# Optimization experiments

Measured on AMD Instinct MI355X. Metric: run time of the kernel, lower is better.

Reference implementation:

```python
import jax, jax.numpy as jnp
import numpy as np

D_MODEL = 128
NUM_HEADS = 8
DEPTH = D_MODEL // NUM_HEADS
NEG = -1e9


def _dense_params(key, d_in, d_out):
    kw, kb = jax.random.split(key)
    # Glorot-uniform like keras Dense default
    lim = np.sqrt(6.0 / (d_in + d_out))
    w = jax.random.uniform(kw, (d_in, d_out), jnp.float32, -lim, lim)
    b = jnp.zeros((d_out,), jnp.float32)
    return w, b


def setup_inputs() -> dict:
    key = jax.random.key(0)
    ks = jax.random.split(key, 16)
    B, N, M, d = 256, 128, 128, D_MODEL
    inp = {
        'x_self': jax.random.normal(ks[0], (B, N, d), jnp.float32),
        'adj_self': jax.random.randint(ks[1], (B, N, N), 0, 2, jnp.int32),
        'mask_self': jnp.ones((B, N), jnp.int32),
        'x_cross': jax.random.normal(ks[2], (B, M, d), jnp.float32),
        'mask_cross': jnp.ones((B, M), jnp.int32),
    }
    names = ['wq_s', 'wk_s', 'wv_s', 'wo_s', 'wq_c', 'wk_c', 'wv_c', 'wo_c']
    for i, nm in enumerate(names):
        w, b = _dense_params(ks[3 + i], d, d)
        inp[nm] = w
        inp['b' + nm[1:]] = b
    wg, bg = _dense_params(ks[12], 3 * d, d)
    inp['wg'] = wg
    inp['bg'] = bg
    return inp


def _split_heads(x):
    B, N, _ = x.shape
    return x.reshape(B, N, NUM_HEADS, DEPTH).transpose(0, 2, 1, 3)  # [B,H,N,depth]


def _merge_heads(x):
    B, H, N, Dp = x.shape
    return x.transpose(0, 2, 1, 3).reshape(B, N, H * Dp)


def _attention(q, k, v, mask, adj=None):
    # q,k,v: [B,H,Nq,depth]; mask: [B,Nk]; adj: [B,Nq,Nk] or None
    logits = jnp.einsum('bhqd,bhkd->bhqk', q, k) / jnp.sqrt(jnp.float32(DEPTH))
    if adj is not None:
        logits = logits + ((1.0 - adj.astype(jnp.float32)) * NEG)[:, None, :, :]
    logits = logits + ((1.0 - mask.astype(jnp.float32)) * NEG)[:, None, None, :]
    w = jax.nn.softmax(logits, axis=-1)
    return jnp.einsum('bhqk,bhkd->bhqd', w, v)


def reference(x_self, adj_self, mask_self, x_cross, mask_cross,
              wq_s, bq_s, wk_s, bk_s, wv_s, bv_s, wo_s, bo_s,
              wq_c, bq_c, wk_c, bk_c, wv_c, bv_c, wo_c, bo_c,
              wg, bg):
    # Self attention (adjacency + padding mask)
    q_s = _split_heads(x_self @ wq_s + bq_s)
    k_s = _split_heads(x_self @ wk_s + bk_s)
    v_s = _split_heads(x_self @ wv_s + bv_s)
    out_s = _merge_heads(_attention(q_s, k_s, v_s, mask_self, adj_self)) @ wo_s + bo_s
    # Cross attention (padding mask only); dropout inactive at inference
    q_c = _split_heads(x_self @ wq_c + bq_c)
    k_c = _split_heads(x_cross @ wk_c + bk_c)
    v_c = _split_heads(x_cross @ wv_c + bv_c)
    out_c = _merge_heads(_attention(q_c, k_c, v_c, mask_cross)) @ wo_c + bo_c
    # Sigmoid gate fusion
    gate = jax.nn.sigmoid(jnp.concatenate([x_self, out_s, out_c], axis=-1) @ wg + bg)
    return (1.0 - gate) * out_s + gate * out_c
```

## Files before the change

### kernel.cpp

```cpp
#include <hip/hip_runtime.h>
#include <hip/hip_bf16.h>

typedef _Float16 f16_t;
typedef __attribute__((ext_vector_type(8))) _Float16 f16x8;
typedef __attribute__((ext_vector_type(4))) float f32x4;

#define LFENCE() asm volatile("" ::: "memory")

__device__ __forceinline__ f16x8 cvt8(const float* p) {
  float4 v0 = *(const float4*)p;
  float4 v1 = *(const float4*)(p + 4);
  f16x8 a;
  a[0] = (f16_t)v0.x; a[1] = (f16_t)v0.y; a[2] = (f16_t)v0.z; a[3] = (f16_t)v0.w;
  a[4] = (f16_t)v1.x; a[5] = (f16_t)v1.y; a[6] = (f16_t)v1.z; a[7] = (f16_t)v1.w;
  return a;
}

__global__ __launch_bounds__(256) void prep_kernel(
    const float* wq_s, const float* wk_s, const float* wv_s,
    const float* wq_c, const float* wk_c, const float* wv_c,
    const float* wo_s, const float* wo_c, const float* wg,
    const float* bos, const float* boc, const float* bgin,
    f16_t* WT, float* bgp)
{
  const int b = blockIdx.x;
  const int tid = threadIdx.x;
  if (b < 11) {
    __shared__ float t[128][129];
    const float* src; f16_t* dst; int ostride;
    switch (b) {
      case 0: src = wq_s; break; case 1: src = wk_s; break;
      case 2: src = wv_s; break; case 3: src = wq_c; break;
      case 4: src = wk_c; break; case 5: src = wv_c; break;
      case 6: src = wo_s; break; case 7: src = wo_c; break;
      default: src = wg + (size_t)(b - 8) * 16384; break;
    }
    if (b < 8) { dst = WT + (size_t)b * 16384; ostride = 128; }
    else       { dst = WT + 8 * 16384 + (b - 8) * 128; ostride = 384; }
#pragma unroll
    for (int i = 0; i < 64; ++i) {
      const int idx = tid + i * 256;
      t[idx & 127][idx >> 7] = src[idx];
    }
    __syncthreads();
#pragma unroll
    for (int i = 0; i < 64; ++i) {
      const int idx = tid + i * 256;
      const int c = idx >> 7, r = idx & 127;
      dst[(size_t)c * ostride + r] = (f16_t)t[c][r];
    }
  } else if (b < 13) {
    const int matsel = b - 11;
    const float* wo = matsel ? wo_c : wo_s;
    const int joff = 128 + matsel * 128;
    f16_t* dst = WT + (size_t)(11 + matsel) * 16384;
    const int wv = tid >> 6, ln = tid & 63, l15 = ln & 15, g = ln >> 4;
    f32x4 acc[2][8];
#pragma unroll
    for (int mm = 0; mm < 2; ++mm)
#pragma unroll
      for (int nt = 0; nt < 8; ++nt) acc[mm][nt] = (f32x4){0.f, 0.f, 0.f, 0.f};
#pragma unroll
    for (int kt = 0; kt < 4; ++kt) {
      f16x8 a[2];
#pragma unroll
      for (int mm = 0; mm < 2; ++mm) {
        const int crow = wv * 32 + mm * 16 + l15;
#pragma unroll
        for (int jj = 0; jj < 8; ++jj)
          a[mm][jj] = (f16_t)wg[(size_t)(joff + kt * 32 + g * 8 + jj) * 128 + crow];
      }
#pragma unroll
      for (int nt = 0; nt < 8; ++nt) {
        f16x8 bf = cvt8(wo + (size_t)(nt * 16 + l15) * 128 + kt * 32 + g * 8);
        acc[0][nt] = __builtin_amdgcn_mfma_f32_16x16x32_f16(a[0], bf, acc[0][nt], 0, 0, 0);
        acc[1][nt] = __builtin_amdgcn_mfma_f32_16x16x32_f16(a[1], bf, acc[1][nt], 0, 0, 0);
      }
    }
#pragma unroll
    for (int mm = 0; mm < 2; ++mm)
#pragma unroll
      for (int nt = 0; nt < 8; ++nt)
#pragma unroll
        for (int r = 0; r < 4; ++r) {
          const int c = wv * 32 + mm * 16 + g * 4 + r;
          dst[(size_t)c * 128 + nt * 16 + l15] = (f16_t)acc[mm][nt][r];
        }
  } else {
    if (tid < 128) {
      float acc = bgin[tid];
      for (int j = 0; j < 128; ++j)
        acc += bos[j] * wg[(size_t)(128 + j) * 128 + tid] +
               boc[j] * wg[(size_t)(256 + j) * 128 + tid];
      bgp[tid] = acc;
    }
  }
}

template <bool TRANSP>
__device__ __forceinline__ void gemm4(
    const f16x8 afr[4], const f16_t* __restrict__ W, const float* __restrict__ bias,
    char* Ob, int l15, int g, int rg, int colbase)
{
  f32x4 acc[4];
#pragma unroll
  for (int nt = 0; nt < 4; ++nt) acc[nt] = (f32x4){0.f, 0.f, 0.f, 0.f};
#pragma unroll
  for (int nt = 0; nt < 4; ++nt)
#pragma unroll
    for (int kt = 0; kt < 4; ++kt) {
      f16x8 b = *(const f16x8*)(W + (size_t)(colbase + nt * 16 + l15) * 128 + kt * 32 + g * 8);
      acc[nt] = __builtin_amdgcn_mfma_f32_16x16x32_f16(afr[kt], b, acc[nt], 0, 0, 0);
    }
#pragma unroll
  for (int nt = 0; nt < 4; ++nt) {
    const int col = colbase + nt * 16 + l15;
    const float bv = bias[col];
#pragma unroll
    for (int r = 0; r < 4; ++r) {
      const int row = rg * 16 + g * 4 + r;
      const f16_t v = (f16_t)(acc[nt][r] + bv);
      if (TRANSP)
        *(f16_t*)(Ob + col * 256 + ((row * 2) ^ ((col & 7) << 4))) = v;
      else
        *(f16_t*)(Ob + row * 256 + ((col * 2) ^ ((row & 7) << 4))) = v;
    }
  }
}

__device__ __forceinline__ void gemmQ(
    const f16x8 afr[4], const f16_t* __restrict__ W, const float* __restrict__ bias,
    char* scr, int l15, int g, int colbase, f16x8 bq[4])
{
  LFENCE();
  f32x4 acc[4];
#pragma unroll
  for (int nt = 0; nt < 4; ++nt) acc[nt] = (f32x4){0.f, 0.f, 0.f, 0.f};
#pragma unroll
  for (int nt = 0; nt < 4; ++nt)
#pragma unroll
    for (int kt = 0; kt < 4; ++kt) {
      f16x8 b = *(const f16x8*)(W + (size_t)(colbase + nt * 16 + l15) * 128 + kt * 32 + g * 8);
      acc[nt] = __builtin_amdgcn_mfma_f32_16x16x32_f16(afr[kt], b, acc[nt], 0, 0, 0);
    }
#pragma unroll
  for (int nt = 0; nt < 4; ++nt) {
    const int col = colbase + nt * 16 + l15;
    const float bv = bias[col];
    const int dloc = nt * 16 + l15;
#pragma unroll
    for (int r = 0; r < 4; ++r) {
      const int qp = g * 4 + r;
      *(f16_t*)(scr + qp * 128 + ((dloc * 2) ^ ((qp & 7) << 4))) = (f16_t)(acc[nt][r] + bv);
    }
  }
  LFENCE();
#pragma unroll
  for (int h = 0; h < 4; ++h) {
    f16x8 z = {0, 0, 0, 0, 0, 0, 0, 0};
    bq[h] = (g < 2)
      ? *(const f16x8*)(scr + l15 * 128 + (((h * 16 + g * 8) * 2) ^ ((l15 & 7) << 4)))
      : z;
  }
  LFENCE();
}

__device__ __forceinline__ void attn_w(
    const char* Kb, const char* Vtb, char* ATTo, char* Pw,
    const f16x8 bq[4], const unsigned aw[4],
    int l15, int g, int rg, int ch)
{
  const f32x4 zero = (f32x4){0.f, 0.f, 0.f, 0.f};
#pragma unroll
  for (int hp = 0; hp < 4; ++hp) {
    const int h = ch * 4 + hp;
    const int d = h * 16 + l15;
    float psum = 0.f;
    f32x4 o = zero;
#pragma unroll
    for (int c = 0; c < 4; ++c) {
      f32x4 st[2];
#pragma unroll
      for (int hf = 0; hf < 2; ++hf) {
        const int krow = (c * 2 + hf) * 16 + l15;
        f16x8 ak = {0, 0, 0, 0, 0, 0, 0, 0};
        if (g < 2)
          ak = *(const f16x8*)(Kb + krow * 256 + (((h * 16 + g * 8) * 2) ^ ((krow & 7) << 4)));
        st[hf] = __builtin_amdgcn_mfma_f32_16x16x32_f16(ak, bq[hp], zero, 0, 0, 0);
      }
#pragma unroll
      for (int hf = 0; hf < 2; ++hf) {
        union { f16_t hh[4]; unsigned long long u; } pk;
#pragma unroll
        for (int r = 0; r < 4; ++r) {
          const int k = (c * 2 + hf) * 16 + g * 4 + r;
          const float e = __expf(st[hf][r] * 0.25f - 4.f);
          const float p = ((aw[k >> 5] >> (k & 31)) & 1u) ? e : 0.f;
          psum += p;
          pk.hh[r] = (f16_t)p;
        }
        *(unsigned long long*)(Pw + l15 * 80 + hf * 32 + g * 8) = pk.u;
      }
      LFENCE();
      union { unsigned long long u[2]; f16x8 v; } pa2;
      pa2.u[0] = *(const unsigned long long*)(Pw + l15 * 80 + g * 16);
      pa2.u[1] = *(const unsigned long long*)(Pw + l15 * 80 + g * 16 + 8);
      LFENCE();
      f16x8 vb = *(const f16x8*)(Vtb + d * 256 + (((c * 32 + g * 8) * 2) ^ ((d & 7) << 4)));
      o = __builtin_amdgcn_mfma_f32_16x16x32_f16(pa2.v, vb, o, 0, 0, 0);
    }
    psum += __shfl_xor(psum, 16);
    psum += __shfl_xor(psum, 32);
    const float inv = 1.f / psum;
#pragma unroll
    for (int r = 0; r < 4; ++r) {
      const float invq = __shfl(inv, g * 4 + r);
      const int row = rg * 16 + g * 4 + r;
      *(f16_t*)(ATTo + row * 256 + (((h * 16 + l15) * 2) ^ ((row & 7) << 4))) =
          (f16_t)(o[r] * invq);
    }
  }
}

__global__ __launch_bounds__(1024) void fused5_kernel(
    const float* __restrict__ Xs_g, const float* __restrict__ Xc_g,
    const int* __restrict__ adj, const int* __restrict__ mask_s,
    const int* __restrict__ mask_c, const f16_t* __restrict__ WT,
    const float* __restrict__ bq_s, const float* __restrict__ bk_s,
    const float* __restrict__ bv_s, const float* __restrict__ bq_c,
    const float* __restrict__ bk_c, const float* __restrict__ bv_c,
    const float* __restrict__ bos, const float* __restrict__ boc,
    const float* __restrict__ bgp, float* __restrict__ OUT)
{
  __shared__ __align__(16) char Kb[32768];
  __shared__ __align__(16) char Vtb[32768];
  __shared__ __align__(16) char ATTs[32768];
  __shared__ __align__(16) char ATTc[32768];
  __shared__ __align__(16) char PR[20480];
  __shared__ unsigned mwS[4], mwC[4];

  const int bb = blockIdx.x;
  const int tid = threadIdx.x;
  const int wv = tid >> 6, ln = tid & 63, l15 = ln & 15, g = ln >> 4;
  const int rg = wv & 7, ch = wv >> 3;
  const int colbase = ch * 64;
  const int arow = rg * 16 + l15;

  if (tid < 512) {
    const int r = tid >> 2, w = tid & 3;
    const int4* ap = (const int4*)(adj + (size_t)bb * 16384 + r * 128 + w * 32);
    unsigned bits = 0;
#pragma unroll
    for (int i = 0; i < 8; ++i) {
      int4 a = ap[i];
      bits |= ((a.x != 0 ? 1u : 0u) | (a.y != 0 ? 2u : 0u) |
               (a.z != 0 ? 4u : 0u) | (a.w != 0 ? 8u : 0u)) << (i * 4);
    }
    *(unsigned*)(ATTc + r * 16 + w * 4) = bits;
  }
  if (wv < 2) {
    unsigned long long bm = __ballot(mask_s[bb * 128 + wv * 64 + ln] != 0);
    if (ln == 0) { mwS[wv * 2] = (unsigned)bm; mwS[wv * 2 + 1] = (unsigned)(bm >> 32); }
  } else if (wv < 4) {
    unsigned long long bm = __ballot(mask_c[bb * 128 + (wv - 2) * 64 + ln] != 0);
    if (ln == 0) { mwC[(wv - 2) * 2] = (unsigned)bm; mwC[(wv - 2) * 2 + 1] = (unsigned)(bm >> 32); }
  }

  f16x8 bqs[4], bqc[4], afrc[4];
  {
    f16x8 afr[4];
#pragma unroll
    for (int kt = 0; kt < 4; ++kt)
      afr[kt] = cvt8(Xs_g + (size_t)bb * 16384 + arow * 128 + kt * 32 + g * 8);
#pragma unroll
    for (int kt = 0; kt < 4; ++kt)
      afrc[kt] = cvt8(Xc_g + (size_t)bb * 16384 + arow * 128 + kt * 32 + g * 8);
    gemm4<false>(afr, WT + 1 * 16384, bk_s, Kb, l15, g, rg, colbase);
    gemm4<true >(afr, WT + 2 * 16384, bv_s, Vtb, l15, g, rg, colbase);
    char* scr = ATTs + wv * 2048;
    gemmQ(afr, WT + 0 * 16384, bq_s, scr, l15, g, colbase, bqs);
    gemmQ(afr, WT + 3 * 16384, bq_c, scr, l15, g, colbase, bqc);
  }
  __syncthreads();

  {
    const uint4 a4 = *(const uint4*)(ATTc + arow * 16);
    unsigned aw[4] = {a4.x & mwS[0], a4.y & mwS[1], a4.z & mwS[2], a4.w & mwS[3]};
    attn_w(Kb, Vtb, ATTs, PR + wv * 1280, bqs, aw, l15, g, rg, ch);
  }
  __syncthreads();

  {
    gemm4<false>(afrc, WT + 4 * 16384, bk_c, Kb, l15, g, rg, colbase);
    gemm4<true >(afrc, WT + 5 * 16384, bv_c, Vtb, l15, g, rg, colbase);
  }
  __syncthreads();

  {
    unsigned aw[4] = {mwC[0], mwC[1], mwC[2], mwC[3]};
    attn_w(Kb, Vtb, ATTc, PR + wv * 1280, bqc, aw, l15, g, rg, ch);
  }
  __syncthreads();

  {
    const int asw = (arow & 7) << 4;
    f16x8 aS[4], aC[4], aX[4];
#pragma unroll
    for (int kt = 0; kt < 4; ++kt) {
      aS[kt] = *(const f16x8*)(ATTs + arow * 256 + ((kt * 64 + g * 16) ^ asw));
      aC[kt] = *(const f16x8*)(ATTc + arow * 256 + ((kt * 64 + g * 16) ^ asw));
      aX[kt] = cvt8(Xs_g + (size_t)bb * 16384 + arow * 128 + kt * 32 + g * 8);
    }
    const f16_t* WoS = WT + 6 * 16384;
    const f16_t* WoC = WT + 7 * 16384;
    const f16_t* Wg1 = WT + 8 * 16384;
    const f16_t* W2p = WT + 11 * 16384;
    const f16_t* W3p = WT + 12 * 16384;
    f32x4 accS[4], accC[4], accG[4];
#pragma unroll
    for (int nt = 0; nt < 4; ++nt) {
      accS[nt] = (f32x4){0.f, 0.f, 0.f, 0.f};
      accC[nt] = (f32x4){0.f, 0.f, 0.f, 0.f};
      accG[nt] = (f32x4){0.f, 0.f, 0.f, 0.f};
    }
#pragma unroll
    for (int nt = 0; nt < 4; ++nt) {
      const size_t col = colbase + nt * 16 + l15;
#pragma unroll
      for (int kt = 0; kt < 4; ++kt) {
        const size_t ko = kt * 32 + g * 8;
        f16x8 bS = *(const f16x8*)(WoS + col * 128 + ko);
        f16x8 bC = *(const f16x8*)(WoC + col * 128 + ko);
        f16x8 bG = *(const f16x8*)(Wg1 + col * 384 + ko);
        f16x8 b2 = *(const f16x8*)(W2p + col * 128 + ko);
        f16x8 b3 = *(const f16x8*)(W3p + col * 128 + ko);
        accS[nt] = __builtin_amdgcn_mfma_f32_16x16x32_f16(aS[kt], bS, accS[nt], 0, 0, 0);
        accC[nt] = __builtin_amdgcn_mfma_f32_16x16x32_f16(aC[kt], bC, accC[nt], 0, 0, 0);
        accG[nt] = __builtin_amdgcn_mfma_f32_16x16x32_f16(aX[kt], bG, accG[nt], 0, 0, 0);
        accG[nt] = __builtin_amdgcn_mfma_f32_16x16x32_f16(aS[kt], b2, accG[nt], 0, 0, 0);
        accG[nt] = __builtin_amdgcn_mfma_f32_16x16x32_f16(aC[kt], b3, accG[nt], 0, 0, 0);
      }
    }
#pragma unroll
    for (int nt = 0; nt < 4; ++nt) {
      const int col = colbase + nt * 16 + l15;
      const float bS = bos[col], bC = boc[col], bG = bgp[col];
#pragma unroll
      for (int r = 0; r < 4; ++r) {
        const int row = rg * 16 + g * 4 + r;
        const float os = accS[nt][r] + bS;
        const float oc = accC[nt][r] + bC;
        const float gv = 1.f / (1.f + __expf(-(accG[nt][r] + bG)));
        OUT[(size_t)bb * 16384 + row * 128 + col] = (1.f - gv) * os + gv * oc;
      }
    }
  }
}

extern "C" void kernel_launch(void* const* d_in, const int* in_sizes, int n_in,
                              void* d_out, int out_size, void* d_ws, size_t ws_size,
                              hipStream_t stream)
{
  const float* x_self  = (const float*)d_in[0];
  const int*   adj     = (const int*)d_in[1];
  const int*   mask_s  = (const int*)d_in[2];
  const float* x_cross = (const float*)d_in[3];
  const int*   mask_c  = (const int*)d_in[4];
  const float* wq_s = (const float*)d_in[5];
  const float* bq_s = (const float*)d_in[6];
  const float* wk_s = (const float*)d_in[7];
  const float* bk_s = (const float*)d_in[8];
  const float* wv_s = (const float*)d_in[9];
  const float* bv_s = (const float*)d_in[10];
  const float* wo_s = (const float*)d_in[11];
  const float* bo_s = (const float*)d_in[12];
  const float* wq_c = (const float*)d_in[13];
  const float* bq_c = (const float*)d_in[14];
  const float* wk_c = (const float*)d_in[15];
  const float* bk_c = (const float*)d_in[16];
  const float* wv_c = (const float*)d_in[17];
  const float* bv_c = (const float*)d_in[18];
  const float* wo_c = (const float*)d_in[19];
  const float* bo_c = (const float*)d_in[20];
  const float* wg   = (const float*)d_in[21];
  const float* bg   = (const float*)d_in[22];
  float* out = (float*)d_out;

  f16_t* WT  = (f16_t*)d_ws;
  float* bgp = (float*)(WT + 13 * 16384);

  prep_kernel<<<14, 256, 0, stream>>>(wq_s, wk_s, wv_s, wq_c, wk_c, wv_c,
                                      wo_s, wo_c, wg, bo_s, bo_c, bg, WT, bgp);
  fused5_kernel<<<256, 1024, 0, stream>>>(x_self, x_cross, adj, mask_s, mask_c, WT,
                                          bq_s, bk_s, bv_s, bq_c, bk_c, bv_c,
                                          bo_s, bo_c, bgp, out);
}
```

Measured before the change: 144.8 us.

## Split fused kernel into parallel self/cross attention and separate output-gate kernel

The single 1024-thread fused kernel ran self and cross attention one after the other per batch. It is replaced by a 512-block attention kernel in which each block handles one batch for either self or cross attention, with 8 waves each doing all 8 heads. That kernel writes fp16 attention outputs to workspace, and a separate 1024-block kernel then does the output projections and the sigmoid gate. The aim is more parallelism, lower LDS use per block (80KB instead of about 150KB) and fewer block-wide barriers. The cost is a global round trip of the fp16 attention results, plus an extra launch.

```diff
diff --git a/kernel.cpp b/kernel.cpp
--- a/kernel.cpp
+++ b/kernel.cpp
@@ -98,23 +98,23 @@
 }
 
 template <bool TRANSP>
-__device__ __forceinline__ void gemm4(
+__device__ __forceinline__ void gemm8(
     const f16x8 afr[4], const f16_t* __restrict__ W, const float* __restrict__ bias,
-    char* Ob, int l15, int g, int rg, int colbase)
-{
-  f32x4 acc[4];
-#pragma unroll
-  for (int nt = 0; nt < 4; ++nt) acc[nt] = (f32x4){0.f, 0.f, 0.f, 0.f};
-#pragma unroll
-  for (int nt = 0; nt < 4; ++nt)
+    char* Ob, int l15, int g, int rg)
+{
+  f32x4 acc[8];
+#pragma unroll
+  for (int nt = 0; nt < 8; ++nt) acc[nt] = (f32x4){0.f, 0.f, 0.f, 0.f};
+#pragma unroll
+  for (int nt = 0; nt < 8; ++nt)
 #pragma unroll
     for (int kt = 0; kt < 4; ++kt) {
-      f16x8 b = *(const f16x8*)(W + (size_t)(colbase + nt * 16 + l15) * 128 + kt * 32 + g * 8);
+      f16x8 b = *(const f16x8*)(W + (size_t)(nt * 16 + l15) * 128 + kt * 32 + g * 8);
       acc[nt] = __builtin_amdgcn_mfma_f32_16x16x32_f16(afr[kt], b, acc[nt], 0, 0, 0);
     }
 #pragma unroll
-  for (int nt = 0; nt < 4; ++nt) {
-    const int col = colbase + nt * 16 + l15;
+  for (int nt = 0; nt < 8; ++nt) {
+    const int col = nt * 16 + l15;
     const float bv = bias[col];
 #pragma unroll
     for (int r = 0; r < 4; ++r) {
@@ -128,52 +128,127 @@
   }
 }
 
-__device__ __forceinline__ void gemmQ(
+__device__ __forceinline__ void gemmQ2(
     const f16x8 afr[4], const f16_t* __restrict__ W, const float* __restrict__ bias,
-    char* scr, int l15, int g, int colbase, f16x8 bq[4])
-{
+    char* scr, int l15, int g, f16x8 bq[8])
+{
+#pragma unroll
+  for (int p = 0; p < 2; ++p) {
+    LFENCE();
+    f32x4 acc[4];
+#pragma unroll
+    for (int nt = 0; nt < 4; ++nt) acc[nt] = (f32x4){0.f, 0.f, 0.f, 0.f};
+#pragma unroll
+    for (int nt = 0; nt < 4; ++nt)
+#pragma unroll
+      for (int kt = 0; kt < 4; ++kt) {
+        f16x8 b = *(const f16x8*)(W + (size_t)(p * 64 + nt * 16 + l15) * 128 + kt * 32 + g * 8);
+        acc[nt] = __builtin_amdgcn_mfma_f32_16x16x32_f16(afr[kt], b, acc[nt], 0, 0, 0);
+      }
+#pragma unroll
+    for (int nt = 0; nt < 4; ++nt) {
+      const float bv = bias[p * 64 + nt * 16 + l15];
+      const int dloc = nt * 16 + l15;
+#pragma unroll
+      for (int r = 0; r < 4; ++r) {
+        const int qp = g * 4 + r;
+        *(f16_t*)(scr + qp * 128 + ((dloc * 2) ^ ((qp & 7) << 4))) = (f16_t)(acc[nt][r] + bv);
+      }
+    }
+    LFENCE();
+#pragma unroll
+    for (int h = 0; h < 4; ++h) {
+      f16x8 z = {0, 0, 0, 0, 0, 0, 0, 0};
+      bq[p * 4 + h] = (g < 2)
+        ? *(const f16x8*)(scr + l15 * 128 + (((h * 16 + g * 8) * 2) ^ ((l15 & 7) << 4)))
+        : z;
+    }
+  }
   LFENCE();
-  f32x4 acc[4];
-#pragma unroll
-  for (int nt = 0; nt < 4; ++nt) acc[nt] = (f32x4){0.f, 0.f, 0.f, 0.f};
-#pragma unroll
-  for (int nt = 0; nt < 4; ++nt)
-#pragma unroll
-    for (int kt = 0; kt < 4; ++kt) {
-      f16x8 b = *(const f16x8*)(W + (size_t)(colbase + nt * 16 + l15) * 128 + kt * 32 + g * 8);
-      acc[nt] = __builtin_amdgcn_mfma_f32_16x16x32_f16(afr[kt], b, acc[nt], 0, 0, 0);
-    }
-#pragma unroll
-  for (int nt = 0; nt < 4; ++nt) {
-    const int col = colbase + nt * 16 + l15;
-    const float bv = bias[col];
-    const int dloc = nt * 16 + l15;
-#pragma unroll
-    for (int r = 0; r < 4; ++r) {
-      const int qp = g * 4 + r;
-      *(f16_t*)(scr + qp * 128 + ((dloc * 2) ^ ((qp & 7) << 4))) = (f16_t)(acc[nt][r] + bv);
-    }
-  }
-  LFENCE();
-#pragma unroll
-  for (int h = 0; h < 4; ++h) {
-    f16x8 z = {0, 0, 0, 0, 0, 0, 0, 0};
-    bq[h] = (g < 2)
-      ? *(const f16x8*)(scr + l15 * 128 + (((h * 16 + g * 8) * 2) ^ ((l15 & 7) << 4)))
-      : z;
-  }
-  LFENCE();
-}
-
-__device__ __forceinline__ void attn_w(
-    const char* Kb, const char* Vtb, char* ATTo, char* Pw,
-    const f16x8 bq[4], const unsigned aw[4],
-    int l15, int g, int rg, int ch)
-{
+}
+
+__global__ __launch_bounds__(512) void battn_kernel(
+    const float* __restrict__ Xs, const float* __restrict__ Xc,
+    const int* __restrict__ adj, const int* __restrict__ mask_s,
+    const int* __restrict__ mask_c, const f16_t* __restrict__ WT,
+    const float* __restrict__ bq_s, const float* __restrict__ bk_s,
+    const float* __restrict__ bv_s, const float* __restrict__ bq_c,
+    const float* __restrict__ bk_c, const float* __restrict__ bv_c,
+    f16_t* __restrict__ att_s, f16_t* __restrict__ att_c)
+{
+  __shared__ __align__(16) char Kb[32768];
+  __shared__ __align__(16) char Vtb[32768];
+  __shared__ __align__(16) char WS[16384];
+
+  const bool self = blockIdx.x < 256;
+  const int bb = blockIdx.x & 255;
+  const int tid = threadIdx.x;
+  const int rg = tid >> 6, ln = tid & 63, l15 = ln & 15, g = ln >> 4;
+  const int arow = rg * 16 + l15;
+  char* scr = WS + rg * 2048;
+
+  const f16_t* WQ = WT + (size_t)(self ? 0 : 3) * 16384;
+  const f16_t* WK = WT + (size_t)(self ? 1 : 4) * 16384;
+  const f16_t* WV = WT + (size_t)(self ? 2 : 5) * 16384;
+  const float* bqv = self ? bq_s : bq_c;
+  const float* bkv = self ? bk_s : bk_c;
+  const float* bvv = self ? bv_s : bv_c;
+  const float* XK  = self ? Xs : Xc;
+  const int* mask  = self ? mask_s : mask_c;
+  f16_t* ATT = self ? att_s : att_c;
+
+  unsigned mw[4];
+  {
+    unsigned long long m0 = __ballot(mask[bb * 128 + ln] != 0);
+    unsigned long long m1 = __ballot(mask[bb * 128 + 64 + ln] != 0);
+    mw[0] = (unsigned)m0; mw[1] = (unsigned)(m0 >> 32);
+    mw[2] = (unsigned)m1; mw[3] = (unsigned)(m1 >> 32);
+  }
+  unsigned aw[4];
+  if (self) {
+    const int row = rg * 16 + (ln & 15);
+    const int w = ln >> 4;
+    const int4* ap = (const int4*)(adj + ((size_t)bb * 128 + row) * 128 + w * 32);
+    unsigned word = 0;
+#pragma unroll
+    for (int i = 0; i < 8; ++i) {
+      int4 a = ap[i];
+      word |= ((a.x != 0 ? 1u : 0u) | (a.y != 0 ? 2u : 0u) |
+               (a.z != 0 ? 4u : 0u) | (a.w != 0 ? 8u : 0u)) << (i * 4);
+    }
+#pragma unroll
+    for (int w2 = 0; w2 < 4; ++w2)
+      aw[w2] = (unsigned)__shfl((int)word, w2 * 16 + l15) & mw[w2];
+  } else {
+#pragma unroll
+    for (int w2 = 0; w2 < 4; ++w2) aw[w2] = mw[w2];
+  }
+
+  f16x8 bq[8];
+  {
+    f16x8 afrK[4];
+#pragma unroll
+    for (int kt = 0; kt < 4; ++kt)
+      afrK[kt] = cvt8(XK + (size_t)bb * 16384 + arow * 128 + kt * 32 + g * 8);
+    gemm8<false>(afrK, WK, bkv, Kb, l15, g, rg);
+    gemm8<true >(afrK, WV, bvv, Vtb, l15, g, rg);
+    f16x8 afrQ[4];
+    if (self) {
+#pragma unroll
+      for (int kt = 0; kt < 4; ++kt) afrQ[kt] = afrK[kt];
+    } else {
+#pragma unroll
+      for (int kt = 0; kt < 4; ++kt)
+        afrQ[kt] = cvt8(Xs + (size_t)bb * 16384 + arow * 128 + kt * 32 + g * 8);
+    }
+    gemmQ2(afrQ, WQ, bqv, scr, l15, g, bq);
+  }
+  __syncthreads();
+
   const f32x4 zero = (f32x4){0.f, 0.f, 0.f, 0.f};
-#pragma unroll
-  for (int hp = 0; hp < 4; ++hp) {
-    const int h = ch * 4 + hp;
+  char* Pw = scr;
+#pragma unroll
+  for (int h = 0; h < 8; ++h) {
     const int d = h * 16 + l15;
     float psum = 0.f;
     f32x4 o = zero;
@@ -186,7 +261,7 @@
         f16x8 ak = {0, 0, 0, 0, 0, 0, 0, 0};
         if (g < 2)
           ak = *(const f16x8*)(Kb + krow * 256 + (((h * 16 + g * 8) * 2) ^ ((krow & 7) << 4)));
-        st[hf] = __builtin_amdgcn_mfma_f32_16x16x32_f16(ak, bq[hp], zero, 0, 0, 0);
+        st[hf] = __builtin_amdgcn_mfma_f32_16x16x32_f16(ak, bq[h], zero, 0, 0, 0);
       }
 #pragma unroll
       for (int hf = 0; hf < 2; ++hf) {
@@ -216,143 +291,68 @@
     for (int r = 0; r < 4; ++r) {
       const float invq = __shfl(inv, g * 4 + r);
       const int row = rg * 16 + g * 4 + r;
-      *(f16_t*)(ATTo + row * 256 + (((h * 16 + l15) * 2) ^ ((row & 7) << 4))) =
-          (f16_t)(o[r] * invq);
-    }
-  }
-}
-
-__global__ __launch_bounds__(1024) void fused5_kernel(
-    const float* __restrict__ Xs_g, const float* __restrict__ Xc_g,
-    const int* __restrict__ adj, const int* __restrict__ mask_s,
-    const int* __restrict__ mask_c, const f16_t* __restrict__ WT,
-    const float* __restrict__ bq_s, const float* __restrict__ bk_s,
-    const float* __restrict__ bv_s, const float* __restrict__ bq_c,
-    const float* __restrict__ bk_c, const float* __restrict__ bv_c,
+      ATT[(size_t)bb * 16384 + row * 128 + h * 16 + l15] = (f16_t)(o[r] * invq);
+    }
+  }
+}
+
+__global__ __launch_bounds__(256) void outgate2_kernel(
+    const f16_t* __restrict__ AS, const f16_t* __restrict__ AC,
+    const float* __restrict__ X, const f16_t* __restrict__ WT,
     const float* __restrict__ bos, const float* __restrict__ boc,
     const float* __restrict__ bgp, float* __restrict__ OUT)
 {
-  __shared__ __align__(16) char Kb[32768];
-  __shared__ __align__(16) char Vtb[32768];
-  __shared__ __align__(16) char ATTs[32768];
-  __shared__ __align__(16) char ATTc[32768];
-  __shared__ __align__(16) char PR[20480];
-  __shared__ unsigned mwS[4], mwC[4];
-
-  const int bb = blockIdx.x;
   const int tid = threadIdx.x;
   const int wv = tid >> 6, ln = tid & 63, l15 = ln & 15, g = ln >> 4;
-  const int rg = wv & 7, ch = wv >> 3;
-  const int colbase = ch * 64;
-  const int arow = rg * 16 + l15;
-
-  if (tid < 512) {
-    const int r = tid >> 2, w = tid & 3;
-    const int4* ap = (const int4*)(adj + (size_t)bb * 16384 + r * 128 + w * 32);
-    unsigned bits = 0;
-#pragma unroll
-    for (int i = 0; i < 8; ++i) {
-      int4 a = ap[i];
-      bits |= ((a.x != 0 ? 1u : 0u) | (a.y != 0 ? 2u : 0u) |
-               (a.z != 0 ? 4u : 0u) | (a.w != 0 ? 8u : 0u)) << (i * 4);
-    }
-    *(unsigned*)(ATTc + r * 16 + w * 4) = bits;
-  }
-  if (wv < 2) {
-    unsigned long long bm = __ballot(mask_s[bb * 128 + wv * 64 + ln] != 0);
-    if (ln == 0) { mwS[wv * 2] = (unsigned)bm; mwS[wv * 2 + 1] = (unsigned)(bm >> 32); }
-  } else if (wv < 4) {
-    unsigned long long bm = __ballot(mask_c[bb * 128 + (wv - 2) * 64 + ln] != 0);
-    if (ln == 0) { mwC[(wv - 2) * 2] = (unsigned)bm; mwC[(wv - 2) * 2 + 1] = (unsigned)(bm >> 32); }
-  }
-
-  f16x8 bqs[4], bqc[4], afrc[4];
-  {
-    f16x8 afr[4];
-#pragma unroll
-    for (int kt = 0; kt < 4; ++kt)
-      afr[kt] = cvt8(Xs_g + (size_t)bb * 16384 + arow * 128 + kt * 32 + g * 8);
-#pragma unroll
-    for (int kt = 0; kt < 4; ++kt)
-      afrc[kt] = cvt8(Xc_g + (size_t)bb * 16384 + arow * 128 + kt * 32 + g * 8);
-    gemm4<false>(afr, WT + 1 * 16384, bk_s, Kb, l15, g, rg, colbase);
-    gemm4<true >(afr, WT + 2 * 16384, bv_s, Vtb, l15, g, rg, colbase);
-    char* scr = ATTs + wv * 2048;
-    gemmQ(afr, WT + 0 * 16384, bq_s, scr, l15, g, colbase, bqs);
-    gemmQ(afr, WT + 3 * 16384, bq_c, scr, l15, g, colbase, bqc);
-  }
-  __syncthreads();
-
-  {
-    const uint4 a4 = *(const uint4*)(ATTc + arow * 16);
-    unsigned aw[4] = {a4.x & mwS[0], a4.y & mwS[1], a4.z & mwS[2], a4.w & mwS[3]};
-    attn_w(Kb, Vtb, ATTs, PR + wv * 1280, bqs, aw, l15, g, rg, ch);
-  }
-  __syncthreads();
-
-  {
-    gemm4<false>(afrc, WT + 4 * 16384, bk_c, Kb, l15, g, rg, colbase);
-    gemm4<true >(afrc, WT + 5 * 16384, bv_c, Vtb, l15, g, rg, colbase);
-  }
-  __syncthreads();
-
-  {
-    unsigned aw[4] = {mwC[0], mwC[1], mwC[2], mwC[3]};
-    attn_w(Kb, Vtb, ATTc, PR + wv * 1280, bqc, aw, l15, g, rg, ch);
-  }
-  __syncthreads();
-
-  {
-    const int asw = (arow & 7) << 4;
-    f16x8 aS[4], aC[4], aX[4];
-#pragma unroll
-    for (int kt = 0; kt < 4; ++kt) {
-      aS[kt] = *(const f16x8*)(ATTs + arow * 256 + ((kt * 64 + g * 16) ^ asw));
-      aC[kt] = *(const f16x8*)(ATTc + arow * 256 + ((kt * 64 + g * 16) ^ asw));
-      aX[kt] = cvt8(Xs_g + (size_t)bb * 16384 + arow * 128 + kt * 32 + g * 8);
-    }
-    const f16_t* WoS = WT + 6 * 16384;
-    const f16_t* WoC = WT + 7 * 16384;
-    const f16_t* Wg1 = WT + 8 * 16384;
-    const f16_t* W2p = WT + 11 * 16384;
-    const f16_t* W3p = WT + 12 * 16384;
-    f32x4 accS[4], accC[4], accG[4];
+  const int rowgrp = wv & 1, colgrp = wv >> 1;
+  const size_t arow = (size_t)blockIdx.x * 32 + rowgrp * 16 + l15;
+  const f16_t* WoS = WT + 6 * 16384;
+  const f16_t* WoC = WT + 7 * 16384;
+  const f16_t* WgT = WT + 8 * 16384;
+  const f16_t* W2T = WT + 11 * 16384;
+  const f16_t* W3T = WT + 12 * 16384;
+
+  f32x4 accS[4], accC[4], accG[4];
+#pragma unroll
+  for (int nt = 0; nt < 4; ++nt) {
+    accS[nt] = (f32x4){0.f, 0.f, 0.f, 0.f};
+    accC[nt] = (f32x4){0.f, 0.f, 0.f, 0.f};
+    accG[nt] = (f32x4){0.f, 0.f, 0.f, 0.f};
+  }
+
+#pragma unroll
+  for (int kt = 0; kt < 4; ++kt) {
+    const size_t ko = kt * 32 + g * 8;
+    f16x8 aS = *(const f16x8*)(AS + arow * 128 + ko);
+    f16x8 aC = *(const f16x8*)(AC + arow * 128 + ko);
+    f16x8 aX = cvt8(X + arow * 128 + ko);
 #pragma unroll
     for (int nt = 0; nt < 4; ++nt) {
-      accS[nt] = (f32x4){0.f, 0.f, 0.f, 0.f};
-      accC[nt] = (f32x4){0.f, 0.f, 0.f, 0.f};
-      accG[nt] = (f32x4){0.f, 0.f, 0.f, 0.f};
-    }
-#pragma unroll
-    for (int nt = 0; nt < 4; ++nt) {
-      const size_t col = colbase + nt * 16 + l15;
-#pragma unroll
-      for (int kt = 0; kt < 4; ++kt) {
-        const size_t ko = kt * 32 + g * 8;
-        f16x8 bS = *(const f16x8*)(WoS + col * 128 + ko);
-        f16x8 bC = *(const f16x8*)(WoC + col * 128 + ko);
-        f16x8 bG = *(const f16x8*)(Wg1 + col * 384 + ko);
-        f16x8 b2 = *(const f16x8*)(W2p + col * 128 + ko);
-        f16x8 b3 = *(const f16x8*)(W3p + col * 128 + ko);
-        accS[nt] = __builtin_amdgcn_mfma_f32_16x16x32_f16(aS[kt], bS, accS[nt], 0, 0, 0);
-        accC[nt] = __builtin_amdgcn_mfma_f32_16x16x32_f16(aC[kt], bC, accC[nt], 0, 0, 0);
-        accG[nt] = __builtin_amdgcn_mfma_f32_16x16x32_f16(aX[kt], bG, accG[nt], 0, 0, 0);
-        accG[nt] = __builtin_amdgcn_mfma_f32_16x16x32_f16(aS[kt], b2, accG[nt], 0, 0, 0);
-        accG[nt] = __builtin_amdgcn_mfma_f32_16x16x32_f16(aC[kt], b3, accG[nt], 0, 0, 0);
-      }
-    }
-#pragma unroll
-    for (int nt = 0; nt < 4; ++nt) {
-      const int col = colbase + nt * 16 + l15;
-      const float bS = bos[col], bC = boc[col], bG = bgp[col];
-#pragma unroll
-      for (int r = 0; r < 4; ++r) {
-        const int row = rg * 16 + g * 4 + r;
-        const float os = accS[nt][r] + bS;
-        const float oc = accC[nt][r] + bC;
-        const float gv = 1.f / (1.f + __expf(-(accG[nt][r] + bG)));
-        OUT[(size_t)bb * 16384 + row * 128 + col] = (1.f - gv) * os + gv * oc;
-      }
+      const size_t col = colgrp * 64 + nt * 16 + l15;
+      f16x8 bS = *(const f16x8*)(WoS + col * 128 + ko);
+      f16x8 bC = *(const f16x8*)(WoC + col * 128 + ko);
+      f16x8 b2 = *(const f16x8*)(W2T + col * 128 + ko);
+      f16x8 b3 = *(const f16x8*)(W3T + col * 128 + ko);
+      f16x8 bX = *(const f16x8*)(WgT + col * 384 + ko);
+      accS[nt] = __builtin_amdgcn_mfma_f32_16x16x32_f16(aS, bS, accS[nt], 0, 0, 0);
+      accC[nt] = __builtin_amdgcn_mfma_f32_16x16x32_f16(aC, bC, accC[nt], 0, 0, 0);
+      accG[nt] = __builtin_amdgcn_mfma_f32_16x16x32_f16(aX, bX, accG[nt], 0, 0, 0);
+      accG[nt] = __builtin_amdgcn_mfma_f32_16x16x32_f16(aS, b2, accG[nt], 0, 0, 0);
+      accG[nt] = __builtin_amdgcn_mfma_f32_16x16x32_f16(aC, b3, accG[nt], 0, 0, 0);
+    }
+  }
+
+  const size_t orow0 = (size_t)blockIdx.x * 32 + rowgrp * 16 + g * 4;
+#pragma unroll
+  for (int nt = 0; nt < 4; ++nt) {
+    const int col = colgrp * 64 + nt * 16 + l15;
+    const float bS = bos[col], bC = boc[col], bG = bgp[col];
+#pragma unroll
+    for (int r = 0; r < 4; ++r) {
+      const float os = accS[nt][r] + bS;
+      const float oc = accC[nt][r] + bC;
+      const float gv = 1.f / (1.f + __expf(-(accG[nt][r] + bG)));
+      OUT[(orow0 + r) * 128 + col] = (1.f - gv) * os + gv * oc;
     }
   }
 }
@@ -386,12 +386,17 @@
   const float* bg   = (const float*)d_in[22];
   float* out = (float*)d_out;
 
+  const size_t SZ = (size_t)256 * 128 * 128;
   f16_t* WT  = (f16_t*)d_ws;
   float* bgp = (float*)(WT + 13 * 16384);
+  f16_t* att_s = (f16_t*)(bgp + 128);
+  f16_t* att_c = att_s + SZ;
 
   prep_kernel<<<14, 256, 0, stream>>>(wq_s, wk_s, wv_s, wq_c, wk_c, wv_c,
                                       wo_s, wo_c, wg, bo_s, bo_c, bg, WT, bgp);
-  fused5_kernel<<<256, 1024, 0, stream>>>(x_self, x_cross, adj, mask_s, mask_c, WT,
-                                          bq_s, bk_s, bv_s, bq_c, bk_c, bv_c,
-                                          bo_s, bo_c, bgp, out);
-}
+  battn_kernel<<<512, 512, 0, stream>>>(x_self, x_cross, adj, mask_s, mask_c, WT,
+                                        bq_s, bk_s, bv_s, bq_c, bk_c, bv_c,
+                                        att_s, att_c);
+  outgate2_kernel<<<1024, 256, 0, stream>>>(att_s, att_c, x_self, WT,
+                                            bo_s, bo_c, bgp, out);
+}
```

Result: faster. 135.5 us (-6.4%).
